# Optimization experiments

Measured on AMD Instinct MI355X. Metric: run time of the kernel, lower is better.

## Reference

```python
import jax, jax.numpy as jnp
import numpy as np

FP4_E2M1_VALUES = jnp.array([0.0, 0.5, 1.0, 1.5, 2.0, 3.0, 4.0, 6.0,
                             -0.0, -0.5, -1.0, -1.5, -2.0, -3.0, -4.0, -6.0],
                            dtype=jnp.float32)

OUT_F, IN_F, BS = 4096, 4096, 16


def setup_inputs() -> dict:
    key = jax.random.key(0)
    k1, k2, k3, k4 = jax.random.split(key, 4)
    x = jax.random.normal(k1, (4, 2048, IN_F), dtype=jnp.float32)
    weight_indices = jax.random.randint(k2, (OUT_F, IN_F // BS, BS), 0, 16, dtype=jnp.int32)
    weight_scales = jax.random.uniform(k3, (OUT_F, IN_F // BS), dtype=jnp.float32)
    bias = jax.random.normal(k4, (OUT_F,), dtype=jnp.float32)
    return {"x": x, "weight_indices": weight_indices,
            "weight_scales": weight_scales, "bias": bias}


def reference(x, weight_indices, weight_scales, bias):
    # Dequantize: gather FP4 values per index, scale per block of 16.
    idx = jnp.clip(weight_indices, 0, 15)              # [O, NB, BS]
    vals = FP4_E2M1_VALUES[idx]                        # [O, NB, BS]
    weight = (vals * weight_scales[:, :, None]).reshape(OUT_F, IN_F)
    # F.linear: y = x @ W^T + b
    return jnp.einsum('bsi,oi->bso', x, weight) + bias
```

## Files before the change

### kernel.cpp

```cpp
#include <hip/hip_runtime.h>
#include <hip/hip_bf16.h>

static constexpr int M_TOT = 8192;
static constexpr int N_TOT = 4096;
static constexpr int K_TOT = 4096;

static constexpr int BM = 256, BN = 256, BK = 32;
static constexpr int NT = K_TOT / BK;
static constexpr int GTHREADS = 512;
static constexpr int BUF_BYTES = 32768;
static constexpr int LDS_BYTES = 4 * BUF_BYTES;

typedef __bf16 bf16x8 __attribute__((ext_vector_type(8)));
typedef float f32x4 __attribute__((ext_vector_type(4)));
typedef unsigned short u16x8 __attribute__((ext_vector_type(8)));

__device__ __forceinline__ unsigned short f2bf(float f) {
  return __builtin_bit_cast(unsigned short, (__bf16)f);
}

__device__ __forceinline__ float fp4_decode(int idx) {
  unsigned u = (unsigned)idx & 15u;
  unsigned sgn = (u >> 3) << 31;
  unsigned mag = u & 7u;
  unsigned e = mag >> 1, m = mag & 1u;
  unsigned bits = (e == 0u) ? (m ? 0x3F000000u : 0u)
                            : (((126u + e) << 23) | (m << 22));
  return __uint_as_float(bits | sgn);
}

__device__ __forceinline__ void glds16(const void* g, void* l) {
  __builtin_amdgcn_global_load_lds(
      (__attribute__((address_space(1))) void*)g,
      (__attribute__((address_space(3))) void*)l, 16, 0, 0);
}

__global__ __launch_bounds__(256) void dequant_w_kernel(
    const int* __restrict__ idx, const float* __restrict__ scales,
    unsigned short* __restrict__ W) {
  const int t = blockIdx.x * 256 + threadIdx.x;
  const int4 v = reinterpret_cast<const int4*>(idx)[t];
  const float s = scales[t >> 2];
  ushort4 o;
  o.x = f2bf(fp4_decode(v.x) * s);
  o.y = f2bf(fp4_decode(v.y) * s);
  o.z = f2bf(fp4_decode(v.z) * s);
  o.w = f2bf(fp4_decode(v.w) * s);
  reinterpret_cast<ushort4*>(W)[t] = o;
}

__global__ __launch_bounds__(256) void convert_x_kernel(
    const float* __restrict__ x, unsigned short* __restrict__ A) {
  const int t = blockIdx.x * 256 + threadIdx.x;
  const float4* xp = reinterpret_cast<const float4*>(x);
  const float4 a = xp[2 * t], b = xp[2 * t + 1];
  u16x8 o;
  o[0] = f2bf(a.x); o[1] = f2bf(a.y); o[2] = f2bf(a.z); o[3] = f2bf(a.w);
  o[4] = f2bf(b.x); o[5] = f2bf(b.y); o[6] = f2bf(b.z); o[7] = f2bf(b.w);
  reinterpret_cast<u16x8*>(A)[t] = o;
}

__global__ __launch_bounds__(GTHREADS, 1) void gemm256(
    const unsigned short* __restrict__ A, const unsigned short* __restrict__ B,
    const float* __restrict__ bias, float* __restrict__ out) {
  extern __shared__ char smem[];

  const int t = threadIdx.x;
  const int lane = t & 63, wid = t >> 6;
  const int wr = wid >> 2;
  const int wc = wid & 3;
  const int ln = lane & 15;
  const int kc = lane >> 4;

  const int bid = blockIdx.x;
  const int bmi = (bid & 7) * 4 + ((bid >> 3) & 3);
  const int bni = bid >> 5;
  const int bm0 = bmi * BM, bn0 = bni * BN;

  const int row_s = t >> 2;
  const int kcd = (t & 3) ^ ((t >> 3) & 3);
  const unsigned short* gA = A + (size_t)(bm0 + row_s) * K_TOT + kcd * 8;
  const unsigned short* gB = B + (size_t)(bn0 + row_s) * K_TOT + kcd * 8;
  char* ldsA = smem + t * 16;
  char* ldsB = smem + 16384 + t * 16;

  const int swz = (kc ^ ((ln >> 1) & 3)) * 16;
  const int base_a = (wr * 128 + ln) * 64 + swz;
  const int base_b = 16384 + (wc * 64 + ln) * 64 + swz;

  f32x4 acc[8][4];
#pragma unroll
  for (int i = 0; i < 8; ++i)
#pragma unroll
    for (int j = 0; j < 4; ++j) acc[i][j] = f32x4{0.f, 0.f, 0.f, 0.f};

  bf16x8 afA[4], afB[4], bfE[4], bfO[4];

#define STAGE_A(kt, bufi) do {                                          \
    const unsigned short* s_ = gA + (size_t)(kt) * BK;                  \
    glds16(s_, ldsA + (bufi) * BUF_BYTES);                              \
    glds16(s_ + (size_t)128 * K_TOT, ldsA + (bufi) * BUF_BYTES + 8192); \
  } while (0)
#define STAGE_B(kt, bufi) do {                                          \
    const unsigned short* s_ = gB + (size_t)(kt) * BK;                  \
    glds16(s_, ldsB + (bufi) * BUF_BYTES);                              \
    glds16(s_ + (size_t)128 * K_TOT, ldsB + (bufi) * BUF_BYTES + 8192); \
  } while (0)

#define READ_AF(dst, bufi, mb) do {                                     \
    const char* p_ = smem + (bufi) * BUF_BYTES + base_a + (mb) * 1024;  \
    dst[0] = *(const bf16x8*)(p_);                                      \
    dst[1] = *(const bf16x8*)(p_ + 1024);                               \
    dst[2] = *(const bf16x8*)(p_ + 2048);                               \
    dst[3] = *(const bf16x8*)(p_ + 3072);                               \
  } while (0)
#define READ_BF(dst, bufi) do {                                         \
    const char* p_ = smem + (bufi) * BUF_BYTES + base_b;                \
    dst[0] = *(const bf16x8*)(p_);                                      \
    dst[1] = *(const bf16x8*)(p_ + 1024);                               \
    dst[2] = *(const bf16x8*)(p_ + 2048);                               \
    dst[3] = *(const bf16x8*)(p_ + 3072);                               \
  } while (0)

#define MFMA16(afs, bfs, mb) do {                                       \
    __builtin_amdgcn_s_setprio(1);                                      \
    _Pragma("unroll")                                                   \
    for (int m_ = 0; m_ < 4; ++m_)                                      \
      _Pragma("unroll")                                                 \
      for (int n_ = 0; n_ < 4; ++n_)                                    \
        acc[(mb) + m_][n_] = __builtin_amdgcn_mfma_f32_16x16x32_bf16(   \
            afs[m_], bfs[n_], acc[(mb) + m_][n_], 0, 0, 0);             \
    __builtin_amdgcn_s_setprio(0);                                      \
  } while (0)

#define VM(n) asm volatile("s_waitcnt vmcnt(" #n ")" ::: "memory")
#define BAR __builtin_amdgcn_s_barrier()

#define PH_A(tt, rb, sb, bfc) do { \
    READ_AF(afB, rb, 4);           \
    STAGE_A((tt) + 3, sb);         \
    MFMA16(afA, bfc, 0);           \
    VM(6); BAR;                    \
  } while (0)
#define PH_B(tt, rbn, sb, bfc, bfn) do { \
    READ_AF(afA, rbn, 0);                \
    READ_BF(bfn, rbn);                   \
    STAGE_B((tt) + 3, sb);               \
    MFMA16(afB, bfc, 4);                 \
    BAR;                                 \
  } while (0)

  STAGE_A(0, 0); STAGE_B(0, 0);
  asm volatile("" ::: "memory");
  STAGE_A(1, 1); STAGE_B(1, 1);
  asm volatile("" ::: "memory");
  STAGE_A(2, 2); STAGE_B(2, 2);
  VM(8);
  BAR;
  READ_AF(afA, 0, 0);
  READ_BF(bfE, 0);

#pragma unroll 1
  for (int tt = 0; tt < NT - 4; tt += 4) {
    PH_A(tt + 0, 0, 3, bfE);
    PH_B(tt + 0, 1, 3, bfE, bfO);
    PH_A(tt + 1, 1, 0, bfO);
    PH_B(tt + 1, 2, 0, bfO, bfE);
    PH_A(tt + 2, 2, 1, bfE);
    PH_B(tt + 2, 3, 1, bfE, bfO);
    PH_A(tt + 3, 3, 2, bfO);
    PH_B(tt + 3, 0, 2, bfO, bfE);
  }

  READ_AF(afB, 0, 4); STAGE_A(127, 3); MFMA16(afA, bfE, 0); VM(6); BAR;
  READ_AF(afA, 1, 0); READ_BF(bfO, 1); STAGE_B(127, 3); MFMA16(afB, bfE, 4); BAR;
  READ_AF(afB, 1, 4); MFMA16(afA, bfO, 0); VM(4); BAR;
  READ_AF(afA, 2, 0); READ_BF(bfE, 2); MFMA16(afB, bfO, 4); BAR;
  READ_AF(afB, 2, 4); MFMA16(afA, bfE, 0); VM(0); BAR;
  READ_AF(afA, 3, 0); READ_BF(bfO, 3); MFMA16(afB, bfE, 4); BAR;
  READ_AF(afB, 3, 4); MFMA16(afA, bfO, 0);
  MFMA16(afB, bfO, 4);

  const int orow0 = bm0 + wr * 128 + (lane >> 4) * 4;
  const int ocol0 = bn0 + wc * 64 + ln;
  float bj[4];
#pragma unroll
  for (int n = 0; n < 4; ++n) bj[n] = bias[ocol0 + n * 16];
#pragma unroll
  for (int mi = 0; mi < 8; ++mi)
#pragma unroll
    for (int n = 0; n < 4; ++n)
#pragma unroll
      for (int q = 0; q < 4; ++q)
        out[(size_t)(orow0 + mi * 16 + q) * N_TOT + ocol0 + n * 16] =
            acc[mi][n][q] + bj[n];
}

extern "C" void kernel_launch(void* const* d_in, const int* in_sizes, int n_in,
                              void* d_out, int out_size, void* d_ws, size_t ws_size,
                              hipStream_t stream) {
  const float* x = (const float*)d_in[0];
  const int* widx = (const int*)d_in[1];
  const float* wsc = (const float*)d_in[2];
  const float* bias = (const float*)d_in[3];
  float* out = (float*)d_out;

  unsigned short* Abf = (unsigned short*)d_ws;
  unsigned short* Wbf = (unsigned short*)((char*)d_ws + (size_t)M_TOT * K_TOT * 2);

  convert_x_kernel<<<dim3((M_TOT * (size_t)K_TOT / 8) / 256), dim3(256), 0, stream>>>(x, Abf);
  dequant_w_kernel<<<dim3((N_TOT * (size_t)K_TOT / 4) / 256), dim3(256), 0, stream>>>(widx, wsc, Wbf);

  (void)hipFuncSetAttribute((const void*)gemm256,
                            hipFuncAttributeMaxDynamicSharedMemorySize, LDS_BYTES);
  gemm256<<<dim3((M_TOT / BM) * (N_TOT / BN)), dim3(GTHREADS), LDS_BYTES, stream>>>(
      Abf, Wbf, bias, out);
}
```

Measured before the change: 279.2 us.

## Fuse fp32-to-bf16 conversion of x into GEMM A-tile loading

Removes the separate convert_x kernel. The GEMM now loads fp32 activations into registers one stage ahead, converts them to bf16 and writes them into swizzled LDS, replacing the direct global-to-LDS async copy for A. This drops a 128 MB read plus 64 MB write-and-reread round trip through global memory and one launch. In exchange, A loads double in bytes per tile (fp32 is re-read by the 16 N-blocks), register pressure rises, and VALU conversion plus LDS writes now sit inside the MFMA pipeline with extra lgkmcnt waits.

```diff
diff --git a/kernel.cpp b/kernel.cpp
--- a/kernel.cpp
+++ b/kernel.cpp
@@ -49,19 +49,8 @@
   reinterpret_cast<ushort4*>(W)[t] = o;
 }
 
-__global__ __launch_bounds__(256) void convert_x_kernel(
-    const float* __restrict__ x, unsigned short* __restrict__ A) {
-  const int t = blockIdx.x * 256 + threadIdx.x;
-  const float4* xp = reinterpret_cast<const float4*>(x);
-  const float4 a = xp[2 * t], b = xp[2 * t + 1];
-  u16x8 o;
-  o[0] = f2bf(a.x); o[1] = f2bf(a.y); o[2] = f2bf(a.z); o[3] = f2bf(a.w);
-  o[4] = f2bf(b.x); o[5] = f2bf(b.y); o[6] = f2bf(b.z); o[7] = f2bf(b.w);
-  reinterpret_cast<u16x8*>(A)[t] = o;
-}
-
 __global__ __launch_bounds__(GTHREADS, 1) void gemm256(
-    const unsigned short* __restrict__ A, const unsigned short* __restrict__ B,
+    const float* __restrict__ X, const unsigned short* __restrict__ B,
     const float* __restrict__ bias, float* __restrict__ out) {
   extern __shared__ char smem[];
 
@@ -79,9 +68,8 @@
 
   const int row_s = t >> 2;
   const int kcd = (t & 3) ^ ((t >> 3) & 3);
-  const unsigned short* gA = A + (size_t)(bm0 + row_s) * K_TOT + kcd * 8;
+  const float* gxA = X + (size_t)(bm0 + row_s) * K_TOT + kcd * 8;
   const unsigned short* gB = B + (size_t)(bn0 + row_s) * K_TOT + kcd * 8;
-  char* ldsA = smem + t * 16;
   char* ldsB = smem + 16384 + t * 16;
 
   const int swz = (kc ^ ((ln >> 1) & 3)) * 16;
@@ -95,12 +83,30 @@
     for (int j = 0; j < 4; ++j) acc[i][j] = f32x4{0.f, 0.f, 0.f, 0.f};
 
   bf16x8 afA[4], afB[4], bfE[4], bfO[4];
-
-#define STAGE_A(kt, bufi) do {                                          \
-    const unsigned short* s_ = gA + (size_t)(kt) * BK;                  \
-    glds16(s_, ldsA + (bufi) * BUF_BYTES);                              \
-    glds16(s_ + (size_t)128 * K_TOT, ldsA + (bufi) * BUF_BYTES + 8192); \
-  } while (0)
+  float4 ldE[4], ldO[4];
+
+#define LD_A(dst, kt) do {                                              \
+    const float* q_ = gxA + (size_t)(kt) * BK;                          \
+    dst[0] = *(const float4*)(q_);                                      \
+    dst[1] = *(const float4*)(q_ + 4);                                  \
+    dst[2] = *(const float4*)(q_ + (size_t)128 * K_TOT);                \
+    dst[3] = *(const float4*)(q_ + (size_t)128 * K_TOT + 4);            \
+  } while (0)
+
+#define WR_A(src, bufi) do {                                            \
+    u16x8 lo_, hi_;                                                     \
+    lo_[0] = f2bf(src[0].x); lo_[1] = f2bf(src[0].y);                   \
+    lo_[2] = f2bf(src[0].z); lo_[3] = f2bf(src[0].w);                   \
+    lo_[4] = f2bf(src[1].x); lo_[5] = f2bf(src[1].y);                   \
+    lo_[6] = f2bf(src[1].z); lo_[7] = f2bf(src[1].w);                   \
+    hi_[0] = f2bf(src[2].x); hi_[1] = f2bf(src[2].y);                   \
+    hi_[2] = f2bf(src[2].z); hi_[3] = f2bf(src[2].w);                   \
+    hi_[4] = f2bf(src[3].x); hi_[5] = f2bf(src[3].y);                   \
+    hi_[6] = f2bf(src[3].z); hi_[7] = f2bf(src[3].w);                   \
+    *reinterpret_cast<u16x8*>(smem + (bufi) * BUF_BYTES + t * 16) = lo_; \
+    *reinterpret_cast<u16x8*>(smem + (bufi) * BUF_BYTES + 8192 + t * 16) = hi_; \
+  } while (0)
+
 #define STAGE_B(kt, bufi) do {                                          \
     const unsigned short* s_ = gB + (size_t)(kt) * BK;                  \
     glds16(s_, ldsB + (bufi) * BUF_BYTES);                              \
@@ -134,13 +140,16 @@
   } while (0)
 
 #define VM(n) asm volatile("s_waitcnt vmcnt(" #n ")" ::: "memory")
+#define LGKM0 asm volatile("s_waitcnt lgkmcnt(0)" ::: "memory")
 #define BAR __builtin_amdgcn_s_barrier()
 
-#define PH_A(tt, rb, sb, bfc) do { \
-    READ_AF(afB, rb, 4);           \
-    STAGE_A((tt) + 3, sb);         \
-    MFMA16(afA, bfc, 0);           \
-    VM(6); BAR;                    \
+#define PH_A(tt, rb, sb, bfc, ldN, ldW) do { \
+    LD_A(ldN, (tt) + 4);       \
+    READ_AF(afB, rb, 4);       \
+    MFMA16(afA, bfc, 0);       \
+    VM(6);                     \
+    WR_A(ldW, sb);             \
+    LGKM0; BAR;                \
   } while (0)
 #define PH_B(tt, rbn, sb, bfc, bfn) do { \
     READ_AF(afA, rbn, 0);                \
@@ -150,31 +159,40 @@
     BAR;                                 \
   } while (0)
 
-  STAGE_A(0, 0); STAGE_B(0, 0);
+  LD_A(ldE, 0); VM(0); WR_A(ldE, 0);
+  LD_A(ldE, 1); VM(0); WR_A(ldE, 1);
+  LD_A(ldE, 2); VM(0); WR_A(ldE, 2);
+  STAGE_B(0, 0);
   asm volatile("" ::: "memory");
-  STAGE_A(1, 1); STAGE_B(1, 1);
+  STAGE_B(1, 1);
   asm volatile("" ::: "memory");
-  STAGE_A(2, 2); STAGE_B(2, 2);
-  VM(8);
+  STAGE_B(2, 2);
+  LD_A(ldO, 3);
+  VM(6);
+  LGKM0;
   BAR;
   READ_AF(afA, 0, 0);
   READ_BF(bfE, 0);
 
 #pragma unroll 1
   for (int tt = 0; tt < NT - 4; tt += 4) {
-    PH_A(tt + 0, 0, 3, bfE);
+    PH_A(tt + 0, 0, 3, bfE, ldE, ldO);
     PH_B(tt + 0, 1, 3, bfE, bfO);
-    PH_A(tt + 1, 1, 0, bfO);
+    PH_A(tt + 1, 1, 0, bfO, ldO, ldE);
     PH_B(tt + 1, 2, 0, bfO, bfE);
-    PH_A(tt + 2, 2, 1, bfE);
+    PH_A(tt + 2, 2, 1, bfE, ldE, ldO);
     PH_B(tt + 2, 3, 1, bfE, bfO);
-    PH_A(tt + 3, 3, 2, bfO);
+    PH_A(tt + 3, 3, 2, bfO, ldO, ldE);
     PH_B(tt + 3, 0, 2, bfO, bfE);
   }
 
-  READ_AF(afB, 0, 4); STAGE_A(127, 3); MFMA16(afA, bfE, 0); VM(6); BAR;
+  READ_AF(afB, 0, 4);
+  MFMA16(afA, bfE, 0);
+  VM(2);
+  WR_A(ldO, 3);
+  LGKM0; BAR;
   READ_AF(afA, 1, 0); READ_BF(bfO, 1); STAGE_B(127, 3); MFMA16(afB, bfE, 4); BAR;
-  READ_AF(afB, 1, 4); MFMA16(afA, bfO, 0); VM(4); BAR;
+  READ_AF(afB, 1, 4); MFMA16(afA, bfO, 0); VM(2); BAR;
   READ_AF(afA, 2, 0); READ_BF(bfE, 2); MFMA16(afB, bfO, 4); BAR;
   READ_AF(afB, 2, 4); MFMA16(afA, bfE, 0); VM(0); BAR;
   READ_AF(afA, 3, 0); READ_BF(bfO, 3); MFMA16(afB, bfE, 4); BAR;
@@ -205,14 +223,13 @@
   const float* bias = (const float*)d_in[3];
   float* out = (float*)d_out;
 
-  unsigned short* Abf = (unsigned short*)d_ws;
-  unsigned short* Wbf = (unsigned short*)((char*)d_ws + (size_t)M_TOT * K_TOT * 2);
-
-  convert_x_kernel<<<dim3((M_TOT * (size_t)K_TOT / 8) / 256), dim3(256), 0, stream>>>(x, Abf);
-  dequant_w_kernel<<<dim3((N_TOT * (size_t)K_TOT / 4) / 256), dim3(256), 0, stream>>>(widx, wsc, Wbf);
+  unsigned short* Wbf = (unsigned short*)d_ws;
+
+  dequant_w_kernel<<<dim3((N_TOT * (size_t)K_TOT / 4) / 256), dim3(256), 0, stream>>>(
+      widx, wsc, Wbf);
 
   (void)hipFuncSetAttribute((const void*)gemm256,
                             hipFuncAttributeMaxDynamicSharedMemorySize, LDS_BYTES);
   gemm256<<<dim3((M_TOT / BM) * (N_TOT / BN)), dim3(GTHREADS), LDS_BYTES, stream>>>(
-      Abf, Wbf, bias, out);
-}
+      x, Wbf, bias, out);
+}
```

After: 429.8 us. +53.9%, slower.
